# Performance work log

Measured on AMD Instinct MI355X. Metric: run time of the kernel, lower is better.

The kernel has to match this reference:

```python
import jax, jax.numpy as jnp
import numpy as np

N, BOND, PHYS = 784, 4, 2
BS = 16384
STD = 1e-08


def setup_inputs() -> dict:
    key = jax.random.key(0)
    k1, k2 = jax.random.split(key)
    data = jax.random.randint(k1, (BS, N), 0, 2).astype(jnp.float32)
    bias = jnp.eye(BOND, dtype=jnp.float32)[:, :, None].repeat(PHYS, axis=2)  # (BOND,BOND,PHYS)
    tensors = STD * jax.random.normal(k2, (N, BOND, BOND, PHYS), dtype=jnp.float32) + bias
    return {"data": data, "tensors": tensors}


def reference(data, tensors):
    # data: (bs, n) in {0,1}; tensors: (n, D, D, P)
    bs, n = data.shape
    emb = jnp.stack([data, 1.0 - data], axis=2)  # (bs, n, P)
    # per-site transfer matrices for every sample: (n, bs, D, D)
    mats = jnp.einsum('nlri,bni->nblr', tensors, emb)
    left0 = mats[0][:, 0, :]  # (bs, D)  -- row 0 of site-0 matrix
    lx0 = jax.nn.log_softmax(tensors[0, 0, 0])  # (P,)

    def step(left, xs):
        t, m = xs  # t: (D, D, P), m: (bs, D, D)
        logits = left @ t[:, 0, :]              # (bs, P)
        lx = jax.nn.log_softmax(logits, axis=1)  # (bs, P)
        new_left = jnp.einsum('bl,blr->br', left, m)
        return new_left, lx

    _, lxs = jax.lax.scan(step, left0, (tensors[1:], mats[1:]))  # (n-1, bs, P)
    logx = jnp.concatenate(
        [jnp.broadcast_to(lx0, (1, bs, PHYS)), lxs], axis=0)  # (n, bs, P)
    logx = jnp.transpose(logx, (1, 0, 2))  # (bs, n, P)
    log_prob = logx[..., 0] * data + logx[..., 1] * (1.0 - data)
    return log_prob.sum(-1)  # (bs,)
```

## Files before the change

### kernel.cpp

```cpp
#include <hip/hip_runtime.h>

#define NSITES 784
#define BS_TOT 16384
#define KSEG 16
#define GSEG 49
#define WPB  64

#define STEP_REG(bitset, c0,c1,c2,c3,c4,c5,c6,c7) do { \
  float p00 = fmaf(left0, c0.x, fmaf(left1, c2.x, fmaf(left2, c4.x, left3 * c6.x))); \
  float p01 = fmaf(left0, c0.y, fmaf(left1, c2.y, fmaf(left2, c4.y, left3 * c6.y))); \
  float p10 = fmaf(left0, c0.z, fmaf(left1, c2.z, fmaf(left2, c4.z, left3 * c6.z))); \
  float p11 = fmaf(left0, c0.w, fmaf(left1, c2.w, fmaf(left2, c4.w, left3 * c6.w))); \
  float p20 = fmaf(left0, c1.x, fmaf(left1, c3.x, fmaf(left2, c5.x, left3 * c7.x))); \
  float p21 = fmaf(left0, c1.y, fmaf(left1, c3.y, fmaf(left2, c5.y, left3 * c7.y))); \
  float p30 = fmaf(left0, c1.z, fmaf(left1, c3.z, fmaf(left2, c5.z, left3 * c7.z))); \
  float p31 = fmaf(left0, c1.w, fmaf(left1, c3.w, fmaf(left2, c5.w, left3 * c7.w))); \
  bool s_ = (bitset); \
  float mx_ = fmaxf(p00, p01); \
  float ch_ = s_ ? p00 : p01; \
  acc_nat += (ch_ - mx_); \
  float ad_ = fabsf(p00 - p01); \
  acc_l2 += __builtin_amdgcn_logf(1.0f + __builtin_amdgcn_exp2f(-ad_ * 1.4426950408889634f)); \
  left0 = s_ ? p00 : p01; \
  left1 = s_ ? p10 : p11; \
  left2 = s_ ? p20 : p21; \
  left3 = s_ ? p30 : p31; \
} while (0)

#define STEP(sbit, TP) do {                                                          \
    const float* t_ = (TP);                                                          \
    float p00 = fmaf(left0, t_[0],  fmaf(left1, t_[8],  fmaf(left2, t_[16], left3 * t_[24]))); \
    float p01 = fmaf(left0, t_[1],  fmaf(left1, t_[9],  fmaf(left2, t_[17], left3 * t_[25]))); \
    float p10 = fmaf(left0, t_[2],  fmaf(left1, t_[10], fmaf(left2, t_[18], left3 * t_[26]))); \
    float p11 = fmaf(left0, t_[3],  fmaf(left1, t_[11], fmaf(left2, t_[19], left3 * t_[27]))); \
    float p20 = fmaf(left0, t_[4],  fmaf(left1, t_[12], fmaf(left2, t_[20], left3 * t_[28]))); \
    float p21 = fmaf(left0, t_[5],  fmaf(left1, t_[13], fmaf(left2, t_[21], left3 * t_[29]))); \
    float p30 = fmaf(left0, t_[6],  fmaf(left1, t_[14], fmaf(left2, t_[22], left3 * t_[30]))); \
    float p31 = fmaf(left0, t_[7],  fmaf(left1, t_[15], fmaf(left2, t_[23], left3 * t_[31]))); \
    bool s_ = (sbit);                                                                \
    float mx_ = fmaxf(p00, p01);                                                     \
    float ch_ = s_ ? p00 : p01;                                                      \
    acc_nat += (ch_ - mx_);                                                          \
    float ad_ = fabsf(p00 - p01);                                                    \
    acc_l2 += __builtin_amdgcn_logf(1.0f + __builtin_amdgcn_exp2f(-ad_ * 1.4426950408889634f)); \
    left0 = s_ ? p00 : p01;                                                          \
    left1 = s_ ? p10 : p11;                                                          \
    left2 = s_ ? p20 : p21;                                                          \
    left3 = s_ ? p30 : p31;                                                          \
} while (0)

#define MM_ROW(Q, Pr) do {                                                           \
    Q.x = fmaf(Pr.x, m0.x, fmaf(Pr.y, m1.x, fmaf(Pr.z, m2.x, Pr.w * m3.x)));         \
    Q.y = fmaf(Pr.x, m0.y, fmaf(Pr.y, m1.y, fmaf(Pr.z, m2.y, Pr.w * m3.y)));         \
    Q.z = fmaf(Pr.x, m0.z, fmaf(Pr.y, m1.z, fmaf(Pr.z, m2.z, Pr.w * m3.z)));         \
    Q.w = fmaf(Pr.x, m0.w, fmaf(Pr.y, m1.w, fmaf(Pr.z, m2.w, Pr.w * m3.w)));         \
} while (0)

__global__ __launch_bounds__(256) void pack_kernel(const float* __restrict__ data,
                                                   unsigned long long* __restrict__ packed) {
    int gid  = blockIdx.x * 256 + threadIdx.x;
    int row  = gid >> 6;
    int lane = threadIdx.x & 63;
    const float* r = data + (size_t)row * NSITES;
    #pragma unroll
    for (int w = 0; w < 12; ++w) {
        unsigned long long m = __ballot(r[w * 64 + lane] == 1.0f);
        if (lane == 0) packed[(size_t)w * BS_TOT + row] = m;
    }
    float v = (lane < 16) ? r[768 + lane] : 0.0f;
    unsigned long long m = __ballot((lane < 16) && (v == 1.0f));
    if (lane == 0) packed[(size_t)12 * BS_TOT + row] = m;
}

__device__ __forceinline__ unsigned long long bit_window(
        const unsigned long long* __restrict__ packed, int n0, int b) {
    int a0 = n0 >> 6, s = n0 & 63;
    unsigned long long w0 = packed[(size_t)a0 * BS_TOT + b];
    unsigned long long w1 = packed[(size_t)(a0 + 1) * BS_TOT + b];
    return s ? ((w0 >> s) | (w1 << (64 - s))) : w0;
}

__global__ __launch_bounds__(256) void phase1_kernel(const float* __restrict__ tensors,
                                                     const unsigned long long* __restrict__ packed,
                                                     float* __restrict__ Pbuf) {
    int b = blockIdx.x * 256 + threadIdx.x;
    int k = blockIdx.y;

    __shared__ __align__(16) float lt[GSEG * 32];
    const float* g = tensors + (size_t)k * GSEG * 32;
    for (int e = threadIdx.x; e < GSEG * 32; e += 256) {
        int i = e >> 5, rem = e & 31;
        int l = rem >> 3, r = (rem >> 1) & 3, p = rem & 1;
        lt[i * 32 + p * 16 + l * 4 + r] = g[e];
    }
    __syncthreads();

    unsigned long long win = bit_window(packed, k * GSEG, b);

    const float4* ms = (const float4*)&lt[(win & 1ull) ? 0 : 16];
    float4 P0 = ms[0], P1 = ms[1], P2 = ms[2], P3 = ms[3];

    #pragma unroll 3
    for (int i = 1; i < GSEG; ++i) {
        const float4* mi = (const float4*)&lt[i * 32 + (((win >> i) & 1ull) ? 0 : 16)];
        float4 m0 = mi[0], m1 = mi[1], m2 = mi[2], m3 = mi[3];
        float4 Q0, Q1, Q2, Q3;
        MM_ROW(Q0, P0); MM_ROW(Q1, P1); MM_ROW(Q2, P2); MM_ROW(Q3, P3);
        P0 = Q0; P1 = Q1; P2 = Q2; P3 = Q3;
    }

    float4* pb = (float4*)(Pbuf + ((size_t)k * BS_TOT + b) * 16);
    pb[0] = P0; pb[1] = P1; pb[2] = P2; pb[3] = P3;
}

__global__ __launch_bounds__(1024, 4) void scan_walk_kernel(
    const float* __restrict__ tensors,
    const unsigned long long* __restrict__ packed,
    const float* __restrict__ Pbuf,
    float* __restrict__ out)
{
    __shared__ __align__(16) float lt[NSITES * 32];
    __shared__ float sPre[KSEG][4][WPB];
    __shared__ float sRes[KSEG][WPB];

    const int t    = threadIdx.x;
    const int wv   = t >> 6;
    const int lane = t & 63;
    const int s0   = blockIdx.x * WPB;
    const int b    = s0 + lane;

    {
        const float4* src = (const float4*)tensors;
        float4* dst = (float4*)lt;
        #pragma unroll
        for (int e = t; e < NSITES * 8; e += 1024) dst[e] = src[e];
    }

    if (wv == 0) {
        float l0 = 1.0f, l1 = 0.0f, l2 = 0.0f, l3 = 0.0f;
        const float4* base = (const float4*)Pbuf + (size_t)b * 4;
        #pragma unroll
        for (int kc = 0; kc < 3; ++kc) {
            float4 R[5][4];
            #pragma unroll
            for (int j = 0; j < 5; ++j) {
                const float4* pb = base + (size_t)(kc * 5 + j) * BS_TOT * 4;
                R[j][0] = pb[0]; R[j][1] = pb[1]; R[j][2] = pb[2]; R[j][3] = pb[3];
            }
            #pragma unroll
            for (int j = 0; j < 5; ++j) {
                const int k = kc * 5 + j;
                sPre[k][0][lane] = l0; sPre[k][1][lane] = l1;
                sPre[k][2][lane] = l2; sPre[k][3][lane] = l3;
                float n0 = fmaf(l0, R[j][0].x, fmaf(l1, R[j][1].x, fmaf(l2, R[j][2].x, l3 * R[j][3].x)));
                float n1 = fmaf(l0, R[j][0].y, fmaf(l1, R[j][1].y, fmaf(l2, R[j][2].y, l3 * R[j][3].y)));
                float n2 = fmaf(l0, R[j][0].z, fmaf(l1, R[j][1].z, fmaf(l2, R[j][2].z, l3 * R[j][3].z)));
                float n3 = fmaf(l0, R[j][0].w, fmaf(l1, R[j][1].w, fmaf(l2, R[j][2].w, l3 * R[j][3].w)));
                l0 = n0; l1 = n1; l2 = n2; l3 = n3;
            }
        }
        sPre[15][0][lane] = l0; sPre[15][1][lane] = l1;
        sPre[15][2][lane] = l2; sPre[15][3][lane] = l3;
    }
    __syncthreads();

    {
        const int k  = wv;
        const int n0 = k * GSEG;
        unsigned long long win = bit_window(packed, n0, b);

        float left0 = sPre[k][0][lane], left1 = sPre[k][1][lane];
        float left2 = sPre[k][2][lane], left3 = sPre[k][3][lane];
        float acc_nat = 0.0f, acc_l2 = 0.0f;

        const float4* tseg = (const float4*)&lt[n0 * 32];
        #pragma unroll 7
        for (int i = 0; i < GSEG; ++i) {
            float4 c0 = tseg[i * 8 + 0], c1 = tseg[i * 8 + 1];
            float4 c2 = tseg[i * 8 + 2], c3 = tseg[i * 8 + 3];
            float4 c4 = tseg[i * 8 + 4], c5 = tseg[i * 8 + 5];
            float4 c6 = tseg[i * 8 + 6], c7 = tseg[i * 8 + 7];
            STEP_REG(((win >> i) & 1ull) != 0, c0,c1,c2,c3,c4,c5,c6,c7);
        }
        sRes[k][lane] = acc_nat - 0.6931471805599453f * acc_l2;
    }
    __syncthreads();

    if (wv == 0) {
        float acc = 0.0f;
        #pragma unroll
        for (int kk = 0; kk < KSEG; ++kk) acc += sRes[kk][lane];
        out[b] = acc;
    }
}

__global__ __launch_bounds__(64) void amps_chain_kernel(
    const float* __restrict__ data, const float* __restrict__ tensors,
    float* __restrict__ out)
{
    int b = blockIdx.x * blockDim.x + threadIdx.x;
    if (b >= BS_TOT) return;
    const float* row = data + (size_t)b * NSITES;
    float left0 = 1.0f, left1 = 0.0f, left2 = 0.0f, left3 = 0.0f;
    float acc_nat = 0.0f, acc_l2 = 0.0f;
    for (int n = 0; n < NSITES; ++n) {
        STEP(row[n] == 1.0f, tensors + (size_t)n * 32);
    }
    out[b] = acc_nat - 0.6931471805599453f * acc_l2;
}

extern "C" void kernel_launch(void* const* d_in, const int* in_sizes, int n_in,
                              void* d_out, int out_size, void* d_ws, size_t ws_size,
                              hipStream_t stream) {
    const float* data    = (const float*)d_in[0];
    const float* tensors = (const float*)d_in[1];
    float* out = (float*)d_out;

    const size_t packed_bytes = (size_t)13 * BS_TOT * 8;
    const size_t Pbuf_bytes   = (size_t)(KSEG - 1) * BS_TOT * 16 * 4;
    const size_t need = packed_bytes + Pbuf_bytes;

    if (ws_size < need) {
        hipLaunchKernelGGL(amps_chain_kernel, dim3(BS_TOT / 64), dim3(64), 0, stream,
                           data, tensors, out);
        return;
    }

    char* wsb = (char*)d_ws;
    unsigned long long* packed = (unsigned long long*)wsb;
    float* Pbuf = (float*)(wsb + packed_bytes);

    hipLaunchKernelGGL(pack_kernel,      dim3((BS_TOT * 64) / 256), dim3(256), 0, stream,
                       data, packed);
    hipLaunchKernelGGL(phase1_kernel,    dim3(BS_TOT / 256, KSEG - 1), dim3(256), 0, stream,
                       tensors, packed, Pbuf);
    hipLaunchKernelGGL(scan_walk_kernel, dim3(BS_TOT / WPB), dim3(1024), 0, stream,
                       tensors, packed, Pbuf, out);
}
```

Measured before the change: 62.93 us.

## Precompute 4-site product tables to shorten segment matrix chains

Adds a kernel that precomputes, for each segment, all 16 bit-pattern products of four consecutive site matrices. The phase-1 segment product then uses 12 table lookups plus one final site instead of 48 sequential 4x4 multiplies, cutting the FMA work and dependency chain length. Separately, the scan-walk kernel stops staging the full tensor array in shared memory and reads site tensors straight from global memory through a wave-uniform pointer, which lowers LDS use and may raise occupancy. The costs are an extra kernel launch and small table builds, plus scalar or global loads in the inner walk loop.

```diff
diff --git a/kernel.cpp b/kernel.cpp
--- a/kernel.cpp
+++ b/kernel.cpp
@@ -4,28 +4,10 @@
 #define BS_TOT 16384
 #define KSEG 16
 #define GSEG 49
+#define NQUAD 12
 #define WPB  64
 
-#define STEP_REG(bitset, c0,c1,c2,c3,c4,c5,c6,c7) do { \
-  float p00 = fmaf(left0, c0.x, fmaf(left1, c2.x, fmaf(left2, c4.x, left3 * c6.x))); \
-  float p01 = fmaf(left0, c0.y, fmaf(left1, c2.y, fmaf(left2, c4.y, left3 * c6.y))); \
-  float p10 = fmaf(left0, c0.z, fmaf(left1, c2.z, fmaf(left2, c4.z, left3 * c6.z))); \
-  float p11 = fmaf(left0, c0.w, fmaf(left1, c2.w, fmaf(left2, c4.w, left3 * c6.w))); \
-  float p20 = fmaf(left0, c1.x, fmaf(left1, c3.x, fmaf(left2, c5.x, left3 * c7.x))); \
-  float p21 = fmaf(left0, c1.y, fmaf(left1, c3.y, fmaf(left2, c5.y, left3 * c7.y))); \
-  float p30 = fmaf(left0, c1.z, fmaf(left1, c3.z, fmaf(left2, c5.z, left3 * c7.z))); \
-  float p31 = fmaf(left0, c1.w, fmaf(left1, c3.w, fmaf(left2, c5.w, left3 * c7.w))); \
-  bool s_ = (bitset); \
-  float mx_ = fmaxf(p00, p01); \
-  float ch_ = s_ ? p00 : p01; \
-  acc_nat += (ch_ - mx_); \
-  float ad_ = fabsf(p00 - p01); \
-  acc_l2 += __builtin_amdgcn_logf(1.0f + __builtin_amdgcn_exp2f(-ad_ * 1.4426950408889634f)); \
-  left0 = s_ ? p00 : p01; \
-  left1 = s_ ? p10 : p11; \
-  left2 = s_ ? p20 : p21; \
-  left3 = s_ ? p30 : p31; \
-} while (0)
+typedef unsigned long long u64;
 
 #define STEP(sbit, TP) do {                                                          \
     const float* t_ = (TP);                                                          \
@@ -56,57 +38,126 @@
     Q.w = fmaf(Pr.x, m0.w, fmaf(Pr.y, m1.w, fmaf(Pr.z, m2.w, Pr.w * m3.w)));         \
 } while (0)
 
+#define MM4(P0,P1,P2,P3) do { float4 Q0,Q1,Q2,Q3; \
+    MM_ROW(Q0,P0); MM_ROW(Q1,P1); MM_ROW(Q2,P2); MM_ROW(Q3,P3); \
+    P0=Q0; P1=Q1; P2=Q2; P3=Q3; } while (0)
+
+__global__ __launch_bounds__(256) void pp_qq_kernel(const float* __restrict__ tensors,
+                                                    float* __restrict__ QQ) {
+    __shared__ float sPP[24][4][16];
+    const int k = blockIdx.x;
+    const int t = threadIdx.x;
+    const int n0 = k * GSEG;
+
+    if (t < 96) {
+        const int j = t >> 2, c2 = t & 3;
+        const float* t0 = tensors + (size_t)(n0 + 2 * j) * 32;
+        const float* t1 = tensors + (size_t)(n0 + 2 * j + 1) * 32;
+        const int p0 = (c2 & 1) ? 0 : 1;
+        const int p1 = (c2 & 2) ? 0 : 1;
+        float A[4][4], B[4][4];
+        #pragma unroll
+        for (int l = 0; l < 4; ++l)
+            #pragma unroll
+            for (int r = 0; r < 4; ++r) {
+                A[l][r] = t0[l * 8 + r * 2 + p0];
+                B[l][r] = t1[l * 8 + r * 2 + p1];
+            }
+        #pragma unroll
+        for (int a = 0; a < 4; ++a)
+            #pragma unroll
+            for (int bb = 0; bb < 4; ++bb)
+                sPP[j][c2][a * 4 + bb] =
+                    fmaf(A[a][0], B[0][bb], fmaf(A[a][1], B[1][bb],
+                    fmaf(A[a][2], B[2][bb], A[a][3] * B[3][bb])));
+    }
+    __syncthreads();
+
+    if (t < 192) {
+        const int q = t >> 4, c = t & 15;
+        const float* A = sPP[2 * q][c & 3];
+        const float* B = sPP[2 * q + 1][(c >> 2) & 3];
+        float* dst = QQ + ((size_t)(k * NQUAD + q) * 16 + c) * 16;
+        #pragma unroll
+        for (int a = 0; a < 4; ++a)
+            #pragma unroll
+            for (int bb = 0; bb < 4; ++bb)
+                dst[a * 4 + bb] =
+                    fmaf(A[a * 4 + 0], B[0 * 4 + bb], fmaf(A[a * 4 + 1], B[1 * 4 + bb],
+                    fmaf(A[a * 4 + 2], B[2 * 4 + bb], A[a * 4 + 3] * B[3 * 4 + bb])));
+    }
+}
+
 __global__ __launch_bounds__(256) void pack_kernel(const float* __restrict__ data,
-                                                   unsigned long long* __restrict__ packed) {
+                                                   u64* __restrict__ packed) {
     int gid  = blockIdx.x * 256 + threadIdx.x;
     int row  = gid >> 6;
     int lane = threadIdx.x & 63;
     const float* r = data + (size_t)row * NSITES;
     #pragma unroll
     for (int w = 0; w < 12; ++w) {
-        unsigned long long m = __ballot(r[w * 64 + lane] == 1.0f);
+        u64 m = __ballot(r[w * 64 + lane] == 1.0f);
         if (lane == 0) packed[(size_t)w * BS_TOT + row] = m;
     }
     float v = (lane < 16) ? r[768 + lane] : 0.0f;
-    unsigned long long m = __ballot((lane < 16) && (v == 1.0f));
+    u64 m = __ballot((lane < 16) && (v == 1.0f));
     if (lane == 0) packed[(size_t)12 * BS_TOT + row] = m;
 }
 
-__device__ __forceinline__ unsigned long long bit_window(
-        const unsigned long long* __restrict__ packed, int n0, int b) {
+__device__ __forceinline__ u64 bit_window(const u64* __restrict__ packed, int n0, int b) {
     int a0 = n0 >> 6, s = n0 & 63;
-    unsigned long long w0 = packed[(size_t)a0 * BS_TOT + b];
-    unsigned long long w1 = packed[(size_t)(a0 + 1) * BS_TOT + b];
+    u64 w0 = packed[(size_t)a0 * BS_TOT + b];
+    u64 w1 = packed[(size_t)(a0 + 1) * BS_TOT + b];
     return s ? ((w0 >> s) | (w1 << (64 - s))) : w0;
 }
 
-__global__ __launch_bounds__(256) void phase1_kernel(const float* __restrict__ tensors,
-                                                     const unsigned long long* __restrict__ packed,
-                                                     float* __restrict__ Pbuf) {
-    int b = blockIdx.x * 256 + threadIdx.x;
-    int k = blockIdx.y;
-
-    __shared__ __align__(16) float lt[GSEG * 32];
-    const float* g = tensors + (size_t)k * GSEG * 32;
-    for (int e = threadIdx.x; e < GSEG * 32; e += 256) {
-        int i = e >> 5, rem = e & 31;
-        int l = rem >> 3, r = (rem >> 1) & 3, p = rem & 1;
-        lt[i * 32 + p * 16 + l * 4 + r] = g[e];
-    }
-    __syncthreads();
-
-    unsigned long long win = bit_window(packed, k * GSEG, b);
-
-    const float4* ms = (const float4*)&lt[(win & 1ull) ? 0 : 16];
-    float4 P0 = ms[0], P1 = ms[1], P2 = ms[2], P3 = ms[3];
-
-    #pragma unroll 3
-    for (int i = 1; i < GSEG; ++i) {
-        const float4* mi = (const float4*)&lt[i * 32 + (((win >> i) & 1ull) ? 0 : 16)];
+__global__ __launch_bounds__(256) void phase1q_kernel(const float* __restrict__ tensors,
+                                                      const u64* __restrict__ packed,
+                                                      const float* __restrict__ QQ,
+                                                      float* __restrict__ Pbuf) {
+    const int b = blockIdx.x * 256 + threadIdx.x;
+    const int k = blockIdx.y;
+    const int n0 = k * GSEG;
+
+    __shared__ __align__(16) float lt[NQUAD * 16 * 20];
+    {
+        const float4* src = (const float4*)(QQ + (size_t)k * NQUAD * 16 * 16);
+        float4* dst = (float4*)lt;
+        for (int e = threadIdx.x; e < NQUAD * 16 * 4; e += 256) {
+            int q = e >> 6, c = (e >> 2) & 15, j = e & 3;
+            dst[q * 80 + c * 5 + j] = src[e];
+        }
+    }
+    __syncthreads();
+
+    u64 win = bit_window(packed, n0, b);
+    const float4* ltf4 = (const float4*)lt;
+
+    float4 P0, P1, P2, P3;
+    {
+        const int c0 = (int)(win & 15ull);
+        const float4* mi = ltf4 + (c0 * 5);
+        P0 = mi[0]; P1 = mi[1]; P2 = mi[2]; P3 = mi[3];
+    }
+    #pragma unroll
+    for (int q = 1; q < NQUAD; ++q) {
+        const int cq = (int)((win >> (4 * q)) & 15ull);
+        const float4* mi = ltf4 + (q * 80 + cq * 5);
         float4 m0 = mi[0], m1 = mi[1], m2 = mi[2], m3 = mi[3];
-        float4 Q0, Q1, Q2, Q3;
-        MM_ROW(Q0, P0); MM_ROW(Q1, P1); MM_ROW(Q2, P2); MM_ROW(Q3, P3);
-        P0 = Q0; P1 = Q1; P2 = Q2; P3 = Q3;
+        MM4(P0, P1, P2, P3);
+    }
+    {
+        const float* t48 = tensors + (size_t)(n0 + 48) * 32;
+        const bool s48 = ((win >> 48) & 1ull) != 0;
+        float4 m0 = make_float4(s48 ? t48[0]  : t48[1],  s48 ? t48[2]  : t48[3],
+                                s48 ? t48[4]  : t48[5],  s48 ? t48[6]  : t48[7]);
+        float4 m1 = make_float4(s48 ? t48[8]  : t48[9],  s48 ? t48[10] : t48[11],
+                                s48 ? t48[12] : t48[13], s48 ? t48[14] : t48[15]);
+        float4 m2 = make_float4(s48 ? t48[16] : t48[17], s48 ? t48[18] : t48[19],
+                                s48 ? t48[20] : t48[21], s48 ? t48[22] : t48[23]);
+        float4 m3 = make_float4(s48 ? t48[24] : t48[25], s48 ? t48[26] : t48[27],
+                                s48 ? t48[28] : t48[29], s48 ? t48[30] : t48[31]);
+        MM4(P0, P1, P2, P3);
     }
 
     float4* pb = (float4*)(Pbuf + ((size_t)k * BS_TOT + b) * 16);
@@ -115,11 +166,10 @@
 
 __global__ __launch_bounds__(1024, 4) void scan_walk_kernel(
     const float* __restrict__ tensors,
-    const unsigned long long* __restrict__ packed,
+    const u64* __restrict__ packed,
     const float* __restrict__ Pbuf,
     float* __restrict__ out)
 {
-    __shared__ __align__(16) float lt[NSITES * 32];
     __shared__ float sPre[KSEG][4][WPB];
     __shared__ float sRes[KSEG][WPB];
 
@@ -128,13 +178,6 @@
     const int lane = t & 63;
     const int s0   = blockIdx.x * WPB;
     const int b    = s0 + lane;
-
-    {
-        const float4* src = (const float4*)tensors;
-        float4* dst = (float4*)lt;
-        #pragma unroll
-        for (int e = t; e < NSITES * 8; e += 1024) dst[e] = src[e];
-    }
 
     if (wv == 0) {
         float l0 = 1.0f, l1 = 0.0f, l2 = 0.0f, l3 = 0.0f;
@@ -167,20 +210,17 @@
     {
         const int k  = wv;
         const int n0 = k * GSEG;
-        unsigned long long win = bit_window(packed, n0, b);
+        u64 win = bit_window(packed, n0, b);
+
+        const int n0u = __builtin_amdgcn_readfirstlane(n0);
+        const float* tb = tensors + (size_t)n0u * 32;
 
         float left0 = sPre[k][0][lane], left1 = sPre[k][1][lane];
         float left2 = sPre[k][2][lane], left3 = sPre[k][3][lane];
         float acc_nat = 0.0f, acc_l2 = 0.0f;
-
-        const float4* tseg = (const float4*)&lt[n0 * 32];
         #pragma unroll 7
         for (int i = 0; i < GSEG; ++i) {
-            float4 c0 = tseg[i * 8 + 0], c1 = tseg[i * 8 + 1];
-            float4 c2 = tseg[i * 8 + 2], c3 = tseg[i * 8 + 3];
-            float4 c4 = tseg[i * 8 + 4], c5 = tseg[i * 8 + 5];
-            float4 c6 = tseg[i * 8 + 6], c7 = tseg[i * 8 + 7];
-            STEP_REG(((win >> i) & 1ull) != 0, c0,c1,c2,c3,c4,c5,c6,c7);
+            STEP(((win >> i) & 1ull) != 0, tb + i * 32);
         }
         sRes[k][lane] = acc_nat - 0.6931471805599453f * acc_l2;
     }
@@ -218,7 +258,8 @@
 
     const size_t packed_bytes = (size_t)13 * BS_TOT * 8;
     const size_t Pbuf_bytes   = (size_t)(KSEG - 1) * BS_TOT * 16 * 4;
-    const size_t need = packed_bytes + Pbuf_bytes;
+    const size_t QQ_bytes     = (size_t)KSEG * NQUAD * 16 * 16 * 4;
+    const size_t need = packed_bytes + Pbuf_bytes + QQ_bytes;
 
     if (ws_size < need) {
         hipLaunchKernelGGL(amps_chain_kernel, dim3(BS_TOT / 64), dim3(64), 0, stream,
@@ -227,13 +268,15 @@
     }
 
     char* wsb = (char*)d_ws;
-    unsigned long long* packed = (unsigned long long*)wsb;
-    float* Pbuf = (float*)(wsb + packed_bytes);
-
+    u64*   packed = (u64*)wsb;
+    float* Pbuf   = (float*)(wsb + packed_bytes);
+    float* QQ     = (float*)(wsb + packed_bytes + Pbuf_bytes);
+
+    hipLaunchKernelGGL(pp_qq_kernel,     dim3(KSEG), dim3(256), 0, stream, tensors, QQ);
     hipLaunchKernelGGL(pack_kernel,      dim3((BS_TOT * 64) / 256), dim3(256), 0, stream,
                        data, packed);
-    hipLaunchKernelGGL(phase1_kernel,    dim3(BS_TOT / 256, KSEG - 1), dim3(256), 0, stream,
-                       tensors, packed, Pbuf);
+    hipLaunchKernelGGL(phase1q_kernel,   dim3(BS_TOT / 256, KSEG - 1), dim3(256), 0, stream,
+                       tensors, packed, QQ, Pbuf);
     hipLaunchKernelGGL(scan_walk_kernel, dim3(BS_TOT / WPB), dim3(1024), 0, stream,
                        tensors, packed, Pbuf, out);
 }
```

New measurement: 55.96 us. 11.1% less time.
